# Performance work log

Measured on AMD Instinct MI355X. Metric: run time of the kernel, lower is better.

## Reference

```python
import jax, jax.numpy as jnp
import numpy as np

B, C, IN_H, IN_W = 32, 16, 64, 64
OUT_H, OUT_W, K, STRIDE = 60, 60, 5, 1


def setup_inputs() -> dict:
    key = jax.random.key(0)
    k1, k2 = jax.random.split(key)
    # spike-like inputs in [0,1)
    in_spikes = jax.random.uniform(k1, (B, C, IN_H, IN_W), dtype=jnp.float32)
    # unshared locally-connected weights: (outH, outW, C_in, K, K, C_out)
    weights = jax.random.normal(k2, (OUT_H, OUT_W, C, K, K, C), dtype=jnp.float32) * (1.0 / (K * K))
    return {"in_spikes": in_spikes, "weights": weights}


def _extract_patches(x, out_h, out_w, k, stride):
    # x: (B, C, H, W) -> patches: (B, C, K, K, out_h, out_w)
    # static K*K loop over kernel offsets (not a data-dim loop)
    rows = []
    for di in range(k):
        cols = []
        for dj in range(k):
            cols.append(x[:, :, di:di + out_h * stride:stride, dj:dj + out_w * stride:stride])
        rows.append(jnp.stack(cols, axis=2))  # (B, C, K, out_h, out_w)
    return jnp.stack(rows, axis=2)  # (B, C, K, K, out_h, out_w)


def reference(in_spikes, weights):
    out_h, out_w, _, k, _, _ = weights.shape
    patches = _extract_patches(in_spikes, out_h, out_w, k, STRIDE)
    # output[b, k_out, i, j] = sum_{c,u,v} patches[b,c,u,v,i,j] * weights[i,j,c,u,v,k_out]
    out = jnp.einsum('bcuvij,ijcuvk->bkij', patches, weights)
    return out
```

## Files before the change

kernel.cpp:

```cpp
#include <hip/hip_runtime.h>
#include <hip/hip_bf16.h>


#define OUT_HW 60
#define IN_HW  64
#define CIN    16
#define COUT   16
#define NPOS   3600
#define BK     512
#define XC_ELE (32u * 64u * 64u * 16u)

typedef __attribute__((ext_vector_type(8))) short bf16x8;
typedef __attribute__((ext_vector_type(4))) float f32x4;

static __device__ __forceinline__ unsigned pk2(float a, float b) {
    union { __hip_bfloat162 h; unsigned u; } cv;
    cv.h = __float22bfloat162_rn(make_float2(a, b));
    return cv.u;
}

__global__ __launch_bounds__(256)
void make_xc(const float* __restrict__ x, ushort* __restrict__ xc) {
    const int bh = blockIdx.x;
    const int b = bh >> 6, h = bh & 63;
    const int t = threadIdx.x;
    const int cq = t & 3, wc = t >> 2;
    const float* src = x + ((size_t)(b * CIN) * IN_HW + h) * IN_HW + wc;
    float f[4];
#pragma unroll
    for (int e = 0; e < 4; ++e)
        f[e] = src[(size_t)(cq * 4 + e) * (IN_HW * IN_HW)];
    union { ushort4 v; unsigned u[2]; } o;
    o.u[0] = pk2(f[0], f[1]);
    o.u[1] = pk2(f[2], f[3]);
    *(ushort4*)&xc[((size_t)bh * IN_HW + wc) * CIN + cq * 4] = o.v;
}

template<int PACKED>
__global__ __launch_bounds__(256, 4)
void lc_pos(const ushort* __restrict__ xc, const float* __restrict__ w,
            float* __restrict__ dst) {
    __shared__ float sWraw[400 * 20];
    __shared__ float sRed[4][32 * 17];

    const int bid = blockIdx.x;
    const int pos = (bid & 7) * 450 + (bid >> 3);
    const int i = pos / OUT_HW, j = pos - i * OUT_HW;
    const int t = threadIdx.x;

    {
        const float4* wf4 = (const float4*)(w + (size_t)pos * 6400);
        float4 vv[7];
#pragma unroll
        for (int it = 0; it < 7; ++it) {
            const int f = t + (it << 8);
            if (f < 1600) vv[it] = wf4[f];
        }
#pragma unroll
        for (int it = 0; it < 7; ++it) {
            const int f = t + (it << 8);
            if (f < 1600) {
                const int m = f >> 2, k4 = (f & 3) << 2;
                *(float4*)&sWraw[m * 20 + k4] = vv[it];
            }
        }
    }
    __syncthreads();

    const int lane = t & 63, wv = t >> 6;
    const int l15 = lane & 15, q = lane >> 4;
    const int qh = q >> 1, c0 = (q & 1) << 3;
    f32x4 acc0 = {0.f, 0.f, 0.f, 0.f}, acc1 = {0.f, 0.f, 0.f, 0.f};
    const int base_hw = i * IN_HW + j;

    for (int cc = wv; cc < 13; cc += 4) {
        const int uvB = cc * 2 + qh;
        const int okB = (uvB < 25);
        float bfv[8];
#pragma unroll
        for (int jj = 0; jj < 8; ++jj) {
            const int c = c0 + jj;
            bfv[jj] = okB ? sWraw[(c * 25 + uvB) * 20 + l15] : 0.f;
        }
        union { bf16x8 v; unsigned u[4]; } pb;
#pragma unroll
        for (int jj = 0; jj < 4; ++jj) pb.u[jj] = pk2(bfv[2 * jj], bfv[2 * jj + 1]);

        const int uvA = okB ? uvB : 24;
        const int uA = (uvA * 13) >> 6;
        const int vA = uvA - 5 * uA;
        const size_t xoff = (size_t)l15 * (IN_HW * IN_HW * CIN)
                          + (size_t)(base_hw + uA * IN_HW + vA) * CIN + c0;
        const bf16x8 a0 = *(const bf16x8*)(xc + xoff);
        const bf16x8 a1 = *(const bf16x8*)(xc + xoff + 16u * IN_HW * IN_HW * CIN);
        acc0 = __builtin_amdgcn_mfma_f32_16x16x32_bf16(a0, pb.v, acc0, 0, 0, 0);
        acc1 = __builtin_amdgcn_mfma_f32_16x16x32_bf16(a1, pb.v, acc1, 0, 0, 0);
    }

#pragma unroll
    for (int r = 0; r < 4; ++r) {
        sRed[wv][(q * 4 + r) * 17 + l15]      = acc0[r];
        sRed[wv][(q * 4 + r + 16) * 17 + l15] = acc1[r];
    }
    __syncthreads();
#pragma unroll
    for (int h = 0; h < 2; ++h) {
        const int o = t + h * 256;
        const int idx = (o >> 4) * 17 + (o & 15);
        const float sv = sRed[0][idx] + sRed[1][idx] + sRed[2][idx] + sRed[3][idx];
        if (PACKED) dst[(size_t)pos * BK + o] = sv;
        else        dst[(size_t)o * NPOS + pos] = sv;
    }
}

__global__ __launch_bounds__(256)
void transpose_out(const float* __restrict__ src, float* __restrict__ out) {
    __shared__ float tile[64][65];
    const int o0 = blockIdx.x * 64;
    const int k0 = blockIdx.y * 64;
    const int t  = threadIdx.x;
    const int tx = t & 63, ty = t >> 6;
    for (int r = ty; r < 64; r += 4) {
        const int oij = o0 + r;
        if (oij < NPOS) tile[r][tx] = src[(size_t)oij * BK + k0 + tx];
    }
    __syncthreads();
    for (int r = ty; r < 64; r += 4) {
        const int oij = o0 + tx;
        if (oij < NPOS) out[(size_t)(k0 + r) * NPOS + oij] = tile[tx][r];
    }
}

__global__ __launch_bounds__(256)
void lc_naive(const float* __restrict__ x, const float* __restrict__ w,
              float* __restrict__ out) {
    const int gid = blockIdx.x * 256 + threadIdx.x;
    if (gid >= 32 * COUT * NPOS) return;
    const int j = gid % OUT_HW;
    int rest = gid / OUT_HW;
    const int i = rest % OUT_HW; rest /= OUT_HW;
    const int k = rest % COUT;
    const int b = rest / COUT;
    const float* wp = w + (size_t)(i * OUT_HW + j) * 6400 + k;
    float s = 0.f;
    for (int c = 0; c < CIN; ++c)
        for (int u = 0; u < 5; ++u)
            for (int v = 0; v < 5; ++v)
                s += x[((size_t)(b * CIN + c) * IN_HW + i + u) * IN_HW + j + v]
                   * wp[((c * 5 + u) * 5 + v) * COUT];
    out[gid] = s;
}

extern "C" void kernel_launch(void* const* d_in, const int* in_sizes, int n_in,
                              void* d_out, int out_size, void* d_ws, size_t ws_size,
                              hipStream_t stream) {
    const float* x = (const float*)d_in[0];
    const float* w = (const float*)d_in[1];
    float* out = (float*)d_out;

    const size_t xcBytes  = (size_t)XC_ELE * 2;
    const size_t outBytes = (size_t)NPOS * BK * 4;
    ushort* xc = (ushort*)d_ws;

    if (ws_size >= xcBytes + outBytes) {
        float* wsOut = (float*)((char*)d_ws + xcBytes);
        make_xc<<<32 * IN_HW, 256, 0, stream>>>(x, xc);
        lc_pos<1><<<NPOS, 256, 0, stream>>>(xc, w, wsOut);
        transpose_out<<<dim3((NPOS + 63) / 64, BK / 64), 256, 0, stream>>>(wsOut, out);
    } else if (ws_size >= xcBytes) {
        make_xc<<<32 * IN_HW, 256, 0, stream>>>(x, xc);
        lc_pos<0><<<NPOS, 256, 0, stream>>>(xc, w, out);
    } else {
        lc_naive<<<(32 * COUT * NPOS + 255) / 256, 256, 0, stream>>>(x, w, out);
    }
}
```

Measured before the change: 190.1 us.

## Load weights via direct global-to-LDS DMA and prefetch activations before barrier

```diff
diff --git a/kernel.cpp b/kernel.cpp
--- a/kernel.cpp
+++ b/kernel.cpp
@@ -17,6 +17,12 @@
     union { __hip_bfloat162 h; unsigned u; } cv;
     cv.h = __float22bfloat162_rn(make_float2(a, b));
     return cv.u;
+}
+
+static __device__ __forceinline__ void g2lds16(const float* g, float* l) {
+    __builtin_amdgcn_global_load_lds(
+        (const __attribute__((address_space(1))) unsigned int*)g,
+        (__attribute__((address_space(3))) unsigned int*)l, 16, 0, 0);
 }
 
 __global__ __launch_bounds__(256)
@@ -40,61 +46,57 @@
 __global__ __launch_bounds__(256, 4)
 void lc_pos(const ushort* __restrict__ xc, const float* __restrict__ w,
             float* __restrict__ dst) {
-    __shared__ float sWraw[400 * 20];
+    __shared__ float sWraw[6400] __attribute__((aligned(16)));
     __shared__ float sRed[4][32 * 17];
 
     const int bid = blockIdx.x;
     const int pos = (bid & 7) * 450 + (bid >> 3);
     const int i = pos / OUT_HW, j = pos - i * OUT_HW;
     const int t = threadIdx.x;
-
-    {
-        const float4* wf4 = (const float4*)(w + (size_t)pos * 6400);
-        float4 vv[7];
-#pragma unroll
-        for (int it = 0; it < 7; ++it) {
-            const int f = t + (it << 8);
-            if (f < 1600) vv[it] = wf4[f];
-        }
-#pragma unroll
-        for (int it = 0; it < 7; ++it) {
-            const int f = t + (it << 8);
-            if (f < 1600) {
-                const int m = f >> 2, k4 = (f & 3) << 2;
-                *(float4*)&sWraw[m * 20 + k4] = vv[it];
-            }
-        }
-    }
-    __syncthreads();
-
     const int lane = t & 63, wv = t >> 6;
     const int l15 = lane & 15, q = lane >> 4;
     const int qh = q >> 1, c0 = (q & 1) << 3;
+
+    const float* wsrc = w + (size_t)pos * 6400 + lane * 4;
+    for (int o = wv; o < 25; o += 4)
+        g2lds16(wsrc + o * 256, &sWraw[o * 256]);
+
+    const int base_hw = i * IN_HW + j;
+    bf16x8 xa0[4], xa1[4];
+#pragma unroll
+    for (int it = 0; it < 4; ++it) {
+        const int cc = wv + it * 4;
+        if (cc < 13) {
+            const int uvB = cc * 2 + qh;
+            const int uvA = (uvB < 25) ? uvB : 24;
+            const int uA = (uvA * 13) >> 6;
+            const int vA = uvA - 5 * uA;
+            const size_t xoff = (size_t)l15 * (IN_HW * IN_HW * CIN)
+                              + (size_t)(base_hw + uA * IN_HW + vA) * CIN + c0;
+            xa0[it] = *(const bf16x8*)(xc + xoff);
+            xa1[it] = *(const bf16x8*)(xc + xoff + 16u * IN_HW * IN_HW * CIN);
+        }
+    }
+
+    __syncthreads();
+
     f32x4 acc0 = {0.f, 0.f, 0.f, 0.f}, acc1 = {0.f, 0.f, 0.f, 0.f};
-    const int base_hw = i * IN_HW + j;
-
-    for (int cc = wv; cc < 13; cc += 4) {
-        const int uvB = cc * 2 + qh;
-        const int okB = (uvB < 25);
-        float bfv[8];
 #pragma unroll
-        for (int jj = 0; jj < 8; ++jj) {
-            const int c = c0 + jj;
-            bfv[jj] = okB ? sWraw[(c * 25 + uvB) * 20 + l15] : 0.f;
+    for (int it = 0; it < 4; ++it) {
+        const int cc = wv + it * 4;
+        if (cc < 13) {
+            const int uvB = cc * 2 + qh;
+            const int okB = (uvB < 25);
+            float bfv[8];
+#pragma unroll
+            for (int jj = 0; jj < 8; ++jj)
+                bfv[jj] = okB ? sWraw[(c0 + jj) * 400 + uvB * 16 + l15] : 0.f;
+            union { bf16x8 v; unsigned u[4]; } pb;
+#pragma unroll
+            for (int jj = 0; jj < 4; ++jj) pb.u[jj] = pk2(bfv[2 * jj], bfv[2 * jj + 1]);
+            acc0 = __builtin_amdgcn_mfma_f32_16x16x32_bf16(xa0[it], pb.v, acc0, 0, 0, 0);
+            acc1 = __builtin_amdgcn_mfma_f32_16x16x32_bf16(xa1[it], pb.v, acc1, 0, 0, 0);
         }
-        union { bf16x8 v; unsigned u[4]; } pb;
-#pragma unroll
-        for (int jj = 0; jj < 4; ++jj) pb.u[jj] = pk2(bfv[2 * jj], bfv[2 * jj + 1]);
-
-        const int uvA = okB ? uvB : 24;
-        const int uA = (uvA * 13) >> 6;
-        const int vA = uvA - 5 * uA;
-        const size_t xoff = (size_t)l15 * (IN_HW * IN_HW * CIN)
-                          + (size_t)(base_hw + uA * IN_HW + vA) * CIN + c0;
-        const bf16x8 a0 = *(const bf16x8*)(xc + xoff);
-        const bf16x8 a1 = *(const bf16x8*)(xc + xoff + 16u * IN_HW * IN_HW * CIN);
-        acc0 = __builtin_amdgcn_mfma_f32_16x16x32_bf16(a0, pb.v, acc0, 0, 0, 0);
-        acc1 = __builtin_amdgcn_mfma_f32_16x16x32_bf16(a1, pb.v, acc1, 0, 0, 0);
     }
 
 #pragma unroll
```

After: 155.1 us. 1.23x faster.
